# Optimization experiments

Measured on AMD Instinct MI355X. Metric: run time of the kernel, lower is better.

Reference implementation:

```python
import jax, jax.numpy as jnp
import numpy as np

N_NODES = 150000  # n_users + n_items
N_EDGES = 2400000
D = 128
LEAKY_SLOPE = 0.2  # tf.nn.leaky_relu default alpha
L2_EPS = 1e-12     # tf.math.l2_normalize epsilon


def setup_inputs() -> dict:
    key = jax.random.key(0)
    ks = jax.random.split(key, 8)
    edge_row = jax.random.randint(ks[0], (N_EDGES,), 0, N_NODES, dtype=jnp.int32)
    edge_col = jax.random.randint(ks[1], (N_EDGES,), 0, N_NODES, dtype=jnp.int32)
    edge_val = jax.random.uniform(ks[2], (N_EDGES,), dtype=jnp.float32)
    ego_embeddings = jax.random.normal(ks[3], (N_NODES, D), dtype=jnp.float32)
    w_gc = jax.random.normal(ks[4], (D, D), dtype=jnp.float32) * 0.05
    b_gc = jax.random.normal(ks[5], (D,), dtype=jnp.float32) * 0.05
    w_bi = jax.random.normal(ks[6], (D, D), dtype=jnp.float32) * 0.05
    b_bi = jax.random.normal(ks[7], (D,), dtype=jnp.float32) * 0.05
    return {"edge_row": edge_row, "edge_col": edge_col, "edge_val": edge_val,
            "ego_embeddings": ego_embeddings,
            "w_gc": w_gc, "b_gc": b_gc, "w_bi": w_bi, "b_bi": b_bi}


def reference(edge_row, edge_col, edge_val, ego_embeddings, w_gc, b_gc, w_bi, b_bi):
    # Sparse A @ ego  (concat over n_fold row-blocks == full SpMM)
    msgs = edge_val[:, None] * ego_embeddings[edge_col]          # [E, D]
    side = jax.ops.segment_sum(msgs, edge_row, num_segments=N_NODES)  # [N, D]
    # dual dense transform + leaky_relu
    sum_emb = jax.nn.leaky_relu(side @ w_gc + b_gc, negative_slope=LEAKY_SLOPE)
    bi_emb = jax.nn.leaky_relu((ego_embeddings * side) @ w_bi + b_bi,
                               negative_slope=LEAKY_SLOPE)
    ego = sum_emb + bi_emb
    # dropout rate = 1 - mess_dropout = 0 -> identity (deterministic)
    # tf.math.l2_normalize(axis=1)
    sq = jnp.sum(ego * ego, axis=1, keepdims=True)
    norm_emb = ego * jax.lax.rsqrt(jnp.maximum(sq, L2_EPS))
    return norm_emb
```

## Files before the change

### kernel.cpp

```cpp
#include <hip/hip_runtime.h>
#include <hip/hip_bf16.h>

constexpr int N_NODES = 150000;
constexpr int N_EDGES = 2400000;
constexpr int D       = 128;
constexpr float LEAKY = 0.2f;
constexpr float L2EPS = 1e-12f;

constexpr int NB_SCAN = (N_NODES + 255) / 256;

constexpr int RB_LOG = 9;
constexpr int RB     = 1 << RB_LOG;
constexpr int NBK    = (N_NODES + RB - 1) >> RB_LOG;
constexpr int EPT_A  = 32;
constexpr int EPB_A  = 256 * EPT_A;

typedef short  short8  __attribute__((ext_vector_type(8)));
typedef short  short4v __attribute__((ext_vector_type(4)));
typedef float  f32x4   __attribute__((ext_vector_type(4)));

static __device__ __forceinline__ short f2bf(float x) {
  __hip_bfloat16 h = __float2bfloat16(x);
  return *reinterpret_cast<short*>(&h);
}

__global__ __launch_bounds__(256) void bucket_hist_kernel(
    const int* __restrict__ erow, int* __restrict__ bkt_cnt) {
  __shared__ int h[NBK];
  const int t = threadIdx.x;
  for (int i = t; i < NBK; i += 256) h[i] = 0;
  __syncthreads();
  const long long e0 = (long long)blockIdx.x * EPB_A;
  #pragma unroll
  for (int k = 0; k < EPT_A; ++k) {
    long long e = e0 + k * 256 + t;
    if (e < N_EDGES) atomicAdd(&h[erow[e] >> RB_LOG], 1);
  }
  __syncthreads();
  for (int i = t; i < NBK; i += 256) {
    int c = h[i];
    if (c) atomicAdd(&bkt_cnt[i], c);
  }
}

__global__ __launch_bounds__(512) void bucket_scan_kernel(
    const int* __restrict__ bkt_cnt,
    int* __restrict__ bbase,
    int* __restrict__ bcur,
    int* __restrict__ offs) {
  __shared__ int s[512];
  const int t = threadIdx.x;
  int v = (t < NBK) ? bkt_cnt[t] : 0;
  s[t] = v;
  __syncthreads();
  for (int off = 1; off < 512; off <<= 1) {
    int tmp = (t >= off) ? s[t - off] : 0;
    __syncthreads();
    s[t] += tmp;
    __syncthreads();
  }
  if (t < NBK) {
    int excl = s[t] - v;
    bbase[t] = excl;
    bcur[t]  = excl;
  }
  if (t == 0) { bbase[NBK] = N_EDGES; offs[N_NODES] = N_EDGES; }
}

__global__ __launch_bounds__(256) void hist_kernel(
    const int* __restrict__ erow, int* __restrict__ cnt) {
  int base = blockIdx.x * 2048 + threadIdx.x;
  #pragma unroll
  for (int k = 0; k < 8; ++k) {
    int e = base + k * 256;
    if (e < N_EDGES) atomicAdd(&cnt[erow[e]], 1);
  }
}

__global__ __launch_bounds__(256) void scan_block_sums(
    const int* __restrict__ cnt, int* __restrict__ bsums) {
  __shared__ int s[256];
  int i = blockIdx.x * 256 + threadIdx.x;
  s[threadIdx.x] = (i < N_NODES) ? cnt[i] : 0;
  __syncthreads();
  for (int off = 128; off > 0; off >>= 1) {
    if (threadIdx.x < off) s[threadIdx.x] += s[threadIdx.x + off];
    __syncthreads();
  }
  if (threadIdx.x == 0) bsums[blockIdx.x] = s[0];
}

__global__ __launch_bounds__(1024) void scan_partials(int* __restrict__ bsums) {
  __shared__ int s[1024];
  int v = (threadIdx.x < NB_SCAN) ? bsums[threadIdx.x] : 0;
  s[threadIdx.x] = v;
  __syncthreads();
  for (int off = 1; off < 1024; off <<= 1) {
    int t = (threadIdx.x >= off) ? s[threadIdx.x - off] : 0;
    __syncthreads();
    s[threadIdx.x] += t;
    __syncthreads();
  }
  if (threadIdx.x < NB_SCAN) bsums[threadIdx.x] = s[threadIdx.x] - v;
}

__global__ __launch_bounds__(256) void scan_final(
    const int* __restrict__ cnt, const int* __restrict__ bsums,
    int* __restrict__ offs, int* __restrict__ cursor) {
  __shared__ int s[256];
  int i = blockIdx.x * 256 + threadIdx.x;
  int v = (i < N_NODES) ? cnt[i] : 0;
  s[threadIdx.x] = v;
  __syncthreads();
  for (int off = 1; off < 256; off <<= 1) {
    int t = (threadIdx.x >= off) ? s[threadIdx.x - off] : 0;
    __syncthreads();
    s[threadIdx.x] += t;
    __syncthreads();
  }
  if (i < N_NODES) {
    int excl = s[threadIdx.x] - v + bsums[blockIdx.x];
    offs[i]   = excl;
    cursor[i] = excl;
  }
  if (i == 0) offs[N_NODES] = N_EDGES;
}

__global__ __launch_bounds__(256) void bucket_scatter_kernel(
    const int*   __restrict__ erow,
    const int*   __restrict__ ecol,
    const float* __restrict__ eval,
    int*         __restrict__ bcur,
    int2*        __restrict__ stage) {
  __shared__ int h[NBK];
  __shared__ int basea[NBK];
  const int t = threadIdx.x;
  const long long e0 = (long long)blockIdx.x * EPB_A;

  for (int i = t; i < NBK; i += 256) h[i] = 0;
  __syncthreads();

  int rows[EPT_A];
  #pragma unroll
  for (int k = 0; k < EPT_A; ++k) {
    long long e = e0 + k * 256 + t;
    int r = -1;
    if (e < N_EDGES) { r = erow[e]; atomicAdd(&h[r >> RB_LOG], 1); }
    rows[k] = r;
  }
  __syncthreads();

  for (int b = t; b < NBK; b += 256) {
    int c = h[b];
    basea[b] = c ? atomicAdd(&bcur[b], c) : 0;
    h[b] = 0;
  }
  __syncthreads();

  #pragma unroll
  for (int k = 0; k < EPT_A; ++k) {
    int r = rows[k];
    if (r >= 0) {
      long long e = e0 + k * 256 + t;
      int bkt  = r >> RB_LOG;
      int rank = atomicAdd(&h[bkt], 1);
      int pos  = basea[bkt] + rank;
      int pack = ecol[e] | ((r & (RB - 1)) << 18);
      stage[pos] = make_int2(pack, __float_as_int(eval[e]));
    }
  }
}

__global__ __launch_bounds__(256) void bucket_permute_kernel(
    const int*  __restrict__ bbase,
    const int2* __restrict__ stage,
    int2*       __restrict__ ev,
    int*        __restrict__ offs) {
  __shared__ int cnt[RB];
  __shared__ int s[256];
  const int t    = threadIdx.x;
  const int bkt  = blockIdx.x;
  const int row0 = bkt << RB_LOG;
  const int w0   = bbase[bkt];
  const int w1   = bbase[bkt + 1];

  for (int i = t; i < RB; i += 256) cnt[i] = 0;
  __syncthreads();

  for (int i = w0 + t; i < w1; i += 256) {
    int px = ((const int*)stage)[2 * (size_t)i];
    atomicAdd(&cnt[(px >> 18) & (RB - 1)], 1);
  }
  __syncthreads();

  int c0 = cnt[2 * t], c1 = cnt[2 * t + 1];
  int pairsum = c0 + c1;
  s[t] = pairsum;
  __syncthreads();
  for (int off = 1; off < 256; off <<= 1) {
    int v = (t >= off) ? s[t - off] : 0;
    __syncthreads();
    s[t] += v;
    __syncthreads();
  }
  int pexcl = s[t] - pairsum;
  int e0 = w0 + pexcl;
  int e1 = e0 + c0;
  cnt[2 * t]     = e0;
  cnt[2 * t + 1] = e1;
  int r0 = row0 + 2 * t;
  if (r0 < N_NODES)     offs[r0]     = e0;
  if (r0 + 1 < N_NODES) offs[r0 + 1] = e1;
  __syncthreads();

  for (int i = w0 + t; i < w1; i += 256) {
    int2 e = stage[i];
    int rl  = (e.x >> 18) & (RB - 1);
    int pos = atomicAdd(&cnt[rl], 1);
    ev[pos] = make_int2(e.x & 0x3FFFF, e.y);
  }
}

__global__ __launch_bounds__(256) void bin_kernel(
    const int*   __restrict__ erow,
    const int*   __restrict__ ecol,
    const float* __restrict__ eval,
    int*         __restrict__ cursor,
    int2*        __restrict__ sorted_ev) {
  int base = blockIdx.x * 1024 + threadIdx.x;
  int e0 = base, e1 = base + 256, e2 = base + 512, e3 = base + 768;
  int r0 = (e0 < N_EDGES) ? erow[e0] : 0;
  int r1 = (e1 < N_EDGES) ? erow[e1] : 0;
  int r2 = (e2 < N_EDGES) ? erow[e2] : 0;
  int r3 = (e3 < N_EDGES) ? erow[e3] : 0;
  int p0 = (e0 < N_EDGES) ? atomicAdd(&cursor[r0], 1) : 0;
  int p1 = (e1 < N_EDGES) ? atomicAdd(&cursor[r1], 1) : 0;
  int p2 = (e2 < N_EDGES) ? atomicAdd(&cursor[r2], 1) : 0;
  int p3 = (e3 < N_EDGES) ? atomicAdd(&cursor[r3], 1) : 0;
  if (e0 < N_EDGES) sorted_ev[p0] = make_int2(ecol[e0], __float_as_int(eval[e0]));
  if (e1 < N_EDGES) sorted_ev[p1] = make_int2(ecol[e1], __float_as_int(eval[e1]));
  if (e2 < N_EDGES) sorted_ev[p2] = make_int2(ecol[e2], __float_as_int(eval[e2]));
  if (e3 < N_EDGES) sorted_ev[p3] = make_int2(ecol[e3], __float_as_int(eval[e3]));
}

__global__ __launch_bounds__(256) void conv_ego_kernel(
    const float* __restrict__ ego, short* __restrict__ ebf) {
  int i = blockIdx.x * 256 + threadIdx.x;
  constexpr int TOTAL = N_NODES * D / 4;
  if (i < TOTAL) {
    float4 v = ((const float4*)ego)[i];
    short4v p;
    p[0] = f2bf(v.x); p[1] = f2bf(v.y); p[2] = f2bf(v.z); p[3] = f2bf(v.w);
    ((short4v*)ebf)[i] = p;
  }
}

__global__ __launch_bounds__(128) void prep_weights_kernel(
    const float* __restrict__ wg, const float* __restrict__ wb,
    short* __restrict__ wtg, short* __restrict__ wtb) {
  int n = blockIdx.x;
  int k = threadIdx.x;
  wtg[n * D + k] = f2bf(wg[k * D + n]);
  wtb[n * D + k] = f2bf(wb[k * D + n]);
}

__global__ __launch_bounds__(256) void spmm_transform_kernel(
    const int*   __restrict__ offs,
    const int2*  __restrict__ ev,
    const short* __restrict__ ebf,
    const float* __restrict__ ego,
    const short* __restrict__ wtg,
    const short* __restrict__ wtb,
    const float* __restrict__ b_gc,
    const float* __restrict__ b_bi,
    float*       __restrict__ out) {
  __shared__ short sA[16][136];
  __shared__ short sP[16][136];
  __shared__ float sO[16][132];
  __shared__ float sInv[16];

  const int t    = threadIdx.x;
  const int g    = t >> 4;
  const int lg   = t & 15;
  const int base = blockIdx.x * 16;
  const int row  = base + g;

  const int s0 = offs[row], s1 = offs[row + 1];
  float a0 = 0.f, a1 = 0.f, a2 = 0.f, a3 = 0.f;
  float a4 = 0.f, a5 = 0.f, a6 = 0.f, a7 = 0.f;

  auto accum = [&](int2 e) {
    uint4 u = *(const uint4*)(ebf + (size_t)e.x * D + lg * 8);
    float v = __int_as_float(e.y);
    a0 = fmaf(v, __uint_as_float(u.x << 16), a0);
    a1 = fmaf(v, __uint_as_float(u.x & 0xffff0000u), a1);
    a2 = fmaf(v, __uint_as_float(u.y << 16), a2);
    a3 = fmaf(v, __uint_as_float(u.y & 0xffff0000u), a3);
    a4 = fmaf(v, __uint_as_float(u.z << 16), a4);
    a5 = fmaf(v, __uint_as_float(u.z & 0xffff0000u), a5);
    a6 = fmaf(v, __uint_as_float(u.w << 16), a6);
    a7 = fmaf(v, __uint_as_float(u.w & 0xffff0000u), a7);
  };

  int i = s0;
  const int n4 = s0 + ((s1 - s0) & ~3);
  for (; i < n4; i += 4) {
    int2 e0 = ev[i], e1 = ev[i + 1], e2 = ev[i + 2], e3 = ev[i + 3];
    accum(e0); accum(e1); accum(e2); accum(e3);
  }
  for (; i < s1; ++i) accum(ev[i]);

  {
    const float* er = ego + (size_t)row * D + lg * 8;
    float4 ev0 = *(const float4*)(er);
    float4 ev1 = *(const float4*)(er + 4);
    short4v pa0, pa1, pp0, pp1;
    pa0[0] = f2bf(a0); pa0[1] = f2bf(a1); pa0[2] = f2bf(a2); pa0[3] = f2bf(a3);
    pa1[0] = f2bf(a4); pa1[1] = f2bf(a5); pa1[2] = f2bf(a6); pa1[3] = f2bf(a7);
    pp0[0] = f2bf(a0 * ev0.x); pp0[1] = f2bf(a1 * ev0.y);
    pp0[2] = f2bf(a2 * ev0.z); pp0[3] = f2bf(a3 * ev0.w);
    pp1[0] = f2bf(a4 * ev1.x); pp1[1] = f2bf(a5 * ev1.y);
    pp1[2] = f2bf(a6 * ev1.z); pp1[3] = f2bf(a7 * ev1.w);
    *(short4v*)&sA[g][lg * 8]     = pa0;
    *(short4v*)&sA[g][lg * 8 + 4] = pa1;
    *(short4v*)&sP[g][lg * 8]     = pp0;
    *(short4v*)&sP[g][lg * 8 + 4] = pp1;
  }
  __syncthreads();

  {
    const int w    = t >> 6;
    const int l64  = t & 63;
    const int arow = l64 & 15;
    const int koff = (l64 >> 4) * 8;
    const int nb   = w * 32;

    f32x4 accg[2] = {{0.f, 0.f, 0.f, 0.f}, {0.f, 0.f, 0.f, 0.f}};
    f32x4 accb[2] = {{0.f, 0.f, 0.f, 0.f}, {0.f, 0.f, 0.f, 0.f}};

    #pragma unroll
    for (int ks = 0; ks < 4; ++ks) {
      const int k0 = ks * 32 + koff;
      short8 a_s = *(const short8*)&sA[arow][k0];
      short8 a_p = *(const short8*)&sP[arow][k0];
      #pragma unroll
      for (int ct = 0; ct < 2; ++ct) {
        const int n = nb + ct * 16 + arow;
        short8 bgf = *(const short8*)(wtg + (size_t)n * D + k0);
        short8 bbf = *(const short8*)(wtb + (size_t)n * D + k0);
        accg[ct] = __builtin_amdgcn_mfma_f32_16x16x32_bf16(a_s, bgf, accg[ct], 0, 0, 0);
        accb[ct] = __builtin_amdgcn_mfma_f32_16x16x32_bf16(a_p, bbf, accb[ct], 0, 0, 0);
      }
    }

    #pragma unroll
    for (int ct = 0; ct < 2; ++ct) {
      const int col = nb + ct * 16 + arow;
      const float bg = b_gc[col];
      const float bb = b_bi[col];
      #pragma unroll
      for (int j = 0; j < 4; ++j) {
        const int r = (l64 >> 4) * 4 + j;
        float x1 = accg[ct][j] + bg; x1 = (x1 > 0.f) ? x1 : LEAKY * x1;
        float x2 = accb[ct][j] + bb; x2 = (x2 > 0.f) ? x2 : LEAKY * x2;
        sO[r][col] = x1 + x2;
      }
    }
  }
  __syncthreads();

  {
    const int r = t >> 4, c16 = t & 15;
    float sum = 0.f;
    #pragma unroll
    for (int i2 = 0; i2 < 8; ++i2) {
      float v = sO[r][c16 * 8 + i2];
      sum = fmaf(v, v, sum);
    }
    #pragma unroll
    for (int off = 8; off > 0; off >>= 1) sum += __shfl_down(sum, off, 16);
    if (c16 == 0) sInv[r] = rsqrtf(fmaxf(sum, L2EPS));
  }
  __syncthreads();

  #pragma unroll
  for (int k = 0; k < 2; ++k) {
    int f  = k * 256 + t;
    int r  = f >> 5;
    int c4 = (f & 31) * 4;
    float inv = sInv[r];
    float4 v = *(const float4*)&sO[r][c4];
    v.x *= inv; v.y *= inv; v.z *= inv; v.w *= inv;
    *(float4*)(out + (size_t)(base + r) * D + c4) = v;
  }
}

__global__ __launch_bounds__(256) void spmm_kernel(
    const int*  __restrict__ offs,
    const int2* __restrict__ ev,
    const float* __restrict__ ego,
    float*       __restrict__ side) {
  const int t = threadIdx.x;
  const int g = t >> 5;
  const int l = t & 31;
  const int row = blockIdx.x * 8 + g;
  if (row >= N_NODES) return;
  const int s0 = offs[row], s1 = offs[row + 1];
  float ax = 0.f, ay = 0.f, az = 0.f, aw = 0.f;
  int i = s0;
  const int n4 = s0 + ((s1 - s0) & ~3);
  for (; i < n4; i += 4) {
    int2 e0 = ev[i], e1 = ev[i + 1], e2 = ev[i + 2], e3 = ev[i + 3];
    float4 g0 = *(const float4*)(ego + (size_t)e0.x * D + 4 * l);
    float4 g1 = *(const float4*)(ego + (size_t)e1.x * D + 4 * l);
    float4 g2 = *(const float4*)(ego + (size_t)e2.x * D + 4 * l);
    float4 g3 = *(const float4*)(ego + (size_t)e3.x * D + 4 * l);
    float v0 = __int_as_float(e0.y), v1 = __int_as_float(e1.y);
    float v2 = __int_as_float(e2.y), v3 = __int_as_float(e3.y);
    ax = fmaf(v0, g0.x, ax); ay = fmaf(v0, g0.y, ay);
    az = fmaf(v0, g0.z, az); aw = fmaf(v0, g0.w, aw);
    ax = fmaf(v1, g1.x, ax); ay = fmaf(v1, g1.y, ay);
    az = fmaf(v1, g1.z, az); aw = fmaf(v1, g1.w, aw);
    ax = fmaf(v2, g2.x, ax); ay = fmaf(v2, g2.y, ay);
    az = fmaf(v2, g2.z, az); aw = fmaf(v2, g2.w, aw);
    ax = fmaf(v3, g3.x, ax); ay = fmaf(v3, g3.y, ay);
    az = fmaf(v3, g3.z, az); aw = fmaf(v3, g3.w, aw);
  }
  for (; i < s1; ++i) {
    int2 e = ev[i];
    float4 gg = *(const float4*)(ego + (size_t)e.x * D + 4 * l);
    float v = __int_as_float(e.y);
    ax = fmaf(v, gg.x, ax); ay = fmaf(v, gg.y, ay);
    az = fmaf(v, gg.z, az); aw = fmaf(v, gg.w, aw);
  }
  *(float4*)(side + (size_t)row * D + 4 * l) = make_float4(ax, ay, az, aw);
}

__global__ __launch_bounds__(256) void transform_mfma_kernel(
    const float* __restrict__ side,
    const float* __restrict__ ego,
    const short* __restrict__ wtg,
    const short* __restrict__ wtb,
    const float* __restrict__ b_gc,
    const float* __restrict__ b_bi,
    float*       __restrict__ out) {
  __shared__ short sA[16][136];
  __shared__ short sP[16][136];
  __shared__ float sO[16][132];
  __shared__ float sInv[16];

  const int t    = threadIdx.x;
  const int w    = t >> 6;
  const int l    = t & 63;
  const int base = blockIdx.x * 16;

  #pragma unroll
  for (int k = 0; k < 2; ++k) {
    int f  = k * 256 + t;
    int r  = f >> 5;
    int c4 = (f & 31) * 4;
    float4 sv = *(const float4*)(side + (size_t)(base + r) * D + c4);
    float4 ev = *(const float4*)(ego  + (size_t)(base + r) * D + c4);
    short4v pa, pp;
    pa[0] = f2bf(sv.x); pa[1] = f2bf(sv.y); pa[2] = f2bf(sv.z); pa[3] = f2bf(sv.w);
    pp[0] = f2bf(sv.x * ev.x); pp[1] = f2bf(sv.y * ev.y);
    pp[2] = f2bf(sv.z * ev.z); pp[3] = f2bf(sv.w * ev.w);
    *(short4v*)&sA[r][c4] = pa;
    *(short4v*)&sP[r][c4] = pp;
  }
  __syncthreads();

  f32x4 accg[2] = {{0.f, 0.f, 0.f, 0.f}, {0.f, 0.f, 0.f, 0.f}};
  f32x4 accb[2] = {{0.f, 0.f, 0.f, 0.f}, {0.f, 0.f, 0.f, 0.f}};

  const int arow = l & 15;
  const int koff = (l >> 4) * 8;
  const int nb   = w * 32;

  #pragma unroll
  for (int ks = 0; ks < 4; ++ks) {
    const int k0 = ks * 32 + koff;
    short8 a_s = *(const short8*)&sA[arow][k0];
    short8 a_p = *(const short8*)&sP[arow][k0];
    #pragma unroll
    for (int ct = 0; ct < 2; ++ct) {
      const int n = nb + ct * 16 + arow;
      short8 bgf = *(const short8*)(wtg + (size_t)n * D + k0);
      short8 bbf = *(const short8*)(wtb + (size_t)n * D + k0);
      accg[ct] = __builtin_amdgcn_mfma_f32_16x16x32_bf16(a_s, bgf, accg[ct], 0, 0, 0);
      accb[ct] = __builtin_amdgcn_mfma_f32_16x16x32_bf16(a_p, bbf, accb[ct], 0, 0, 0);
    }
  }

  #pragma unroll
  for (int ct = 0; ct < 2; ++ct) {
    const int col = nb + ct * 16 + arow;
    const float bg = b_gc[col];
    const float bb = b_bi[col];
    #pragma unroll
    for (int j = 0; j < 4; ++j) {
      const int r = (l >> 4) * 4 + j;
      float x1 = accg[ct][j] + bg; x1 = (x1 > 0.f) ? x1 : LEAKY * x1;
      float x2 = accb[ct][j] + bb; x2 = (x2 > 0.f) ? x2 : LEAKY * x2;
      sO[r][col] = x1 + x2;
    }
  }
  __syncthreads();

  {
    const int r = t >> 4, c16 = t & 15;
    float sum = 0.f;
    #pragma unroll
    for (int i = 0; i < 8; ++i) {
      float v = sO[r][c16 * 8 + i];
      sum = fmaf(v, v, sum);
    }
    #pragma unroll
    for (int off = 8; off > 0; off >>= 1) sum += __shfl_down(sum, off, 16);
    if (c16 == 0) sInv[r] = rsqrtf(fmaxf(sum, L2EPS));
  }
  __syncthreads();

  #pragma unroll
  for (int k = 0; k < 2; ++k) {
    int f  = k * 256 + t;
    int r  = f >> 5;
    int c4 = (f & 31) * 4;
    float inv = sInv[r];
    float4 v = *(const float4*)&sO[r][c4];
    v.x *= inv; v.y *= inv; v.z *= inv; v.w *= inv;
    *(float4*)(out + (size_t)(base + r) * D + c4) = v;
  }
}

__global__ __launch_bounds__(256) void scatter_kernel(
    const int*   __restrict__ erow,
    const int*   __restrict__ ecol,
    const float* __restrict__ eval,
    const float* __restrict__ ego,
    float*       __restrict__ side) {
  long long t = (long long)blockIdx.x * blockDim.x + threadIdx.x;
  int e = (int)(t >> 5);
  if (e >= N_EDGES) return;
  int c = (int)(t & 31);
  int r  = erow[e];
  int cl = ecol[e];
  float v = eval[e];
  const float4* src = (const float4*)(ego + (long long)cl * D);
  float4 m = src[c];
  float* dst = side + (long long)r * D + c * 4;
  atomicAdd(dst + 0, v * m.x);
  atomicAdd(dst + 1, v * m.y);
  atomicAdd(dst + 2, v * m.z);
  atomicAdd(dst + 3, v * m.w);
}

__global__ __launch_bounds__(128) void transform_f32_kernel(
    const float* __restrict__ side,
    const float* __restrict__ ego,
    const float* __restrict__ w_gc,
    const float* __restrict__ b_gc,
    const float* __restrict__ w_bi,
    const float* __restrict__ b_bi,
    float*       __restrict__ out) {
  constexpr int RPB = 16;
  __shared__ float s_side[RPB][D];
  __shared__ float s_prod[RPB][D];
  __shared__ float s_part[RPB][2];
  const int j    = threadIdx.x;
  const int base = blockIdx.x * RPB;
  #pragma unroll
  for (int r = 0; r < RPB; ++r) {
    int node = base + r;
    float s = 0.f, e = 0.f;
    if (node < N_NODES) {
      s = side[(long long)node * D + j];
      e = ego [(long long)node * D + j];
    }
    s_side[r][j] = s;
    s_prod[r][j] = e * s;
  }
  __syncthreads();
  float acc_gc[RPB], acc_bi[RPB];
  #pragma unroll
  for (int r = 0; r < RPB; ++r) { acc_gc[r] = 0.f; acc_bi[r] = 0.f; }
  for (int k = 0; k < D; ++k) {
    float wg = w_gc[k * D + j];
    float wb = w_bi[k * D + j];
    #pragma unroll
    for (int r = 0; r < RPB; ++r) {
      acc_gc[r] = fmaf(s_side[r][k], wg, acc_gc[r]);
      acc_bi[r] = fmaf(s_prod[r][k], wb, acc_bi[r]);
    }
  }
  const float bg = b_gc[j];
  const float bb = b_bi[j];
  #pragma unroll
  for (int r = 0; r < RPB; ++r) {
    float x1 = acc_gc[r] + bg; x1 = (x1 > 0.f) ? x1 : LEAKY * x1;
    float x2 = acc_bi[r] + bb; x2 = (x2 > 0.f) ? x2 : LEAKY * x2;
    acc_gc[r] = x1 + x2;
  }
  const int lane = j & 63;
  const int wv   = j >> 6;
  #pragma unroll
  for (int r = 0; r < RPB; ++r) {
    float sq = acc_gc[r] * acc_gc[r];
    #pragma unroll
    for (int off = 32; off > 0; off >>= 1) sq += __shfl_down(sq, off, 64);
    if (lane == 0) s_part[r][wv] = sq;
  }
  __syncthreads();
  #pragma unroll
  for (int r = 0; r < RPB; ++r) {
    int node = base + r;
    if (node < N_NODES) {
      float tot = s_part[r][0] + s_part[r][1];
      float inv = rsqrtf(fmaxf(tot, L2EPS));
      out[(long long)node * D + j] = acc_gc[r] * inv;
    }
  }
}

extern "C" void kernel_launch(void* const* d_in, const int* in_sizes, int n_in,
                              void* d_out, int out_size, void* d_ws, size_t ws_size,
                              hipStream_t stream) {
  const int*   erow = (const int*)  d_in[0];
  const int*   ecol = (const int*)  d_in[1];
  const float* eval = (const float*)d_in[2];
  const float* ego  = (const float*)d_in[3];
  const float* w_gc = (const float*)d_in[4];
  const float* b_gc = (const float*)d_in[5];
  const float* w_bi = (const float*)d_in[6];
  const float* b_bi = (const float*)d_in[7];
  float* out = (float*)d_out;

  auto align256 = [](size_t x) { return (x + 255) & ~(size_t)255; };
  size_t off_cnt    = 0;
  size_t off_offs   = align256(off_cnt    + (size_t)N_NODES * 4);
  size_t off_cursor = align256(off_offs   + (size_t)(N_NODES + 1) * 4);
  size_t off_bsums  = align256(off_cursor + (size_t)N_NODES * 4);
  size_t off_bcur   = align256(off_bsums  + 1024 * 4);
  size_t off_wtg    = align256(off_bcur   + (size_t)NBK * 4);
  size_t off_wtb    = align256(off_wtg    + (size_t)D * D * 2);
  size_t off_ev     = align256(off_wtb    + (size_t)D * D * 2);
  size_t off_ebf    = align256(off_ev     + (size_t)N_EDGES * 8);
  size_t ws_mid     = off_ebf;
  size_t ws_sort    = off_ebf + (size_t)N_EDGES * 8;
  size_t ws_full    = off_ebf + (size_t)N_NODES * D * 2;

  if (ws_size >= ws_mid) {
    char* ws = (char*)d_ws;
    int*   cnt    = (int*)  (ws + off_cnt);
    int*   offs   = (int*)  (ws + off_offs);
    int*   cursor = (int*)  (ws + off_cursor);
    int*   bsums  = (int*)  (ws + off_bsums);
    int*   bcur   = (int*)  (ws + off_bcur);
    short* wtg    = (short*)(ws + off_wtg);
    short* wtb    = (short*)(ws + off_wtb);
    int2*  ev     = (int2*) (ws + off_ev);
    short* ebf    = (short*)(ws + off_ebf);
    int2*  stage  = (int2*) (ws + off_ebf);

    bool bucketed = (ws_size >= ws_sort);
    if (bucketed) {
      hipMemsetAsync(cnt, 0, (size_t)NBK * 4, stream);
      bucket_hist_kernel<<<(N_EDGES + EPB_A - 1) / EPB_A, 256, 0, stream>>>(erow, cnt);
      bucket_scan_kernel<<<1, 512, 0, stream>>>(cnt, bsums, bcur, offs);
      bucket_scatter_kernel<<<(N_EDGES + EPB_A - 1) / EPB_A, 256, 0, stream>>>(
          erow, ecol, eval, bcur, stage);
      bucket_permute_kernel<<<NBK, 256, 0, stream>>>(bsums, stage, ev, offs);
    } else {
      hipMemsetAsync(cnt, 0, (size_t)N_NODES * 4, stream);
      hist_kernel<<<(N_EDGES + 2047) / 2048, 256, 0, stream>>>(erow, cnt);
      scan_block_sums<<<NB_SCAN, 256, 0, stream>>>(cnt, bsums);
      scan_partials<<<1, 1024, 0, stream>>>(bsums);
      scan_final<<<NB_SCAN, 256, 0, stream>>>(cnt, bsums, offs, cursor);
      bin_kernel<<<(N_EDGES + 1023) / 1024, 256, 0, stream>>>(
          erow, ecol, eval, cursor, ev);
    }
    prep_weights_kernel<<<D, D, 0, stream>>>(w_gc, w_bi, wtg, wtb);

    if (ws_size >= ws_full) {
      conv_ego_kernel<<<(N_NODES * D / 4 + 255) / 256, 256, 0, stream>>>(ego, ebf);
      spmm_transform_kernel<<<N_NODES / 16, 256, 0, stream>>>(
          offs, ev, ebf, ego, wtg, wtb, b_gc, b_bi, out);
    } else {
      float* side = out;
      spmm_kernel<<<(N_NODES + 7) / 8, 256, 0, stream>>>(offs, ev, ego, side);
      transform_mfma_kernel<<<N_NODES / 16, 256, 0, stream>>>(
          side, ego, wtg, wtb, b_gc, b_bi, out);
    }
  } else {
    float* side = out;
    hipMemsetAsync(side, 0, (size_t)N_NODES * D * 4, stream);
    long long total = (long long)N_EDGES * 32;
    int grid = (int)((total + 255) / 256);
    scatter_kernel<<<grid, 256, 0, stream>>>(erow, ecol, eval, ego, side);
    transform_f32_kernel<<<N_NODES / 16, 128, 0, stream>>>(
        side, ego, w_gc, b_gc, w_bi, b_bi, out);
  }
}
```

Measured before the change: 409.8 us.

## Balance fused SpMM edges across 16-row block with LDS atomic row reduction

The fused SpMM+transform kernel now splits the block's total edge range evenly across its 16 thread groups instead of giving each group one row. Row identity is kept in the packed edge word, and partial sums are flushed into shared memory with atomics whenever the row changes. This targets load imbalance from varying row degrees, at the cost of LDS zeroing, extra syncs, atomic flushes and masking of the column index.

New measurement: 483.7 us. +18.0%, slower.

```diff
diff --git a/kernel.cpp b/kernel.cpp
--- a/kernel.cpp
+++ b/kernel.cpp
@@ -217,7 +217,7 @@
     int2 e = stage[i];
     int rl  = (e.x >> 18) & (RB - 1);
     int pos = atomicAdd(&cnt[rl], 1);
-    ev[pos] = make_int2(e.x & 0x3FFFF, e.y);
+    ev[pos] = e;
   }
 }
 
@@ -283,15 +283,36 @@
   const int g    = t >> 4;
   const int lg   = t & 15;
   const int base = blockIdx.x * 16;
-  const int row  = base + g;
-
-  const int s0 = offs[row], s1 = offs[row + 1];
+
+  #pragma unroll
+  for (int k = 0; k < 8; ++k) {
+    int idx = k * 256 + t;
+    sO[idx >> 7][idx & 127] = 0.f;
+  }
+  __syncthreads();
+
+  const int W0 = offs[base], W1 = offs[base + 16];
+  const int chunk = ((W1 - W0) + 15) >> 4;
+  const int cbeg = W0 + g * chunk;
+  const int cend = min(cbeg + chunk, W1);
+
+  const short* ebl = ebf + lg * 8;
+
   float a0 = 0.f, a1 = 0.f, a2 = 0.f, a3 = 0.f;
   float a4 = 0.f, a5 = 0.f, a6 = 0.f, a7 = 0.f;
-
-  auto accum = [&](int2 e) {
-    uint4 u = *(const uint4*)(ebf + (size_t)e.x * D + lg * 8);
-    float v = __int_as_float(e.y);
+  int cur = -1;
+
+  auto flush = [&]() {
+    if (cur >= 0) {
+      float* dst = &sO[cur][lg * 8];
+      atomicAdd(dst + 0, a0); atomicAdd(dst + 1, a1);
+      atomicAdd(dst + 2, a2); atomicAdd(dst + 3, a3);
+      atomicAdd(dst + 4, a4); atomicAdd(dst + 5, a5);
+      atomicAdd(dst + 6, a6); atomicAdd(dst + 7, a7);
+    }
+    a0 = a1 = a2 = a3 = a4 = a5 = a6 = a7 = 0.f;
+  };
+  auto accum = [&](uint4 u, float v) {
     a0 = fmaf(v, __uint_as_float(u.x << 16), a0);
     a1 = fmaf(v, __uint_as_float(u.x & 0xffff0000u), a1);
     a2 = fmaf(v, __uint_as_float(u.y << 16), a2);
@@ -302,25 +323,49 @@
     a7 = fmaf(v, __uint_as_float(u.w & 0xffff0000u), a7);
   };
 
-  int i = s0;
-  const int n4 = s0 + ((s1 - s0) & ~3);
+  int i = cbeg;
+  const int n4 = cbeg + ((cend - cbeg) & ~3);
   for (; i < n4; i += 4) {
-    int2 e0 = ev[i], e1 = ev[i + 1], e2 = ev[i + 2], e3 = ev[i + 3];
-    accum(e0); accum(e1); accum(e2); accum(e3);
-  }
-  for (; i < s1; ++i) accum(ev[i]);
+    int2 e0 = ev[i + 0], e1 = ev[i + 1], e2 = ev[i + 2], e3 = ev[i + 3];
+    uint4 u0 = *(const uint4*)(ebl + (size_t)(e0.x & 0x3FFFF) * D);
+    uint4 u1 = *(const uint4*)(ebl + (size_t)(e1.x & 0x3FFFF) * D);
+    uint4 u2 = *(const uint4*)(ebl + (size_t)(e2.x & 0x3FFFF) * D);
+    uint4 u3 = *(const uint4*)(ebl + (size_t)(e3.x & 0x3FFFF) * D);
+    int r0 = (e0.x >> 18) & 15, r1 = (e1.x >> 18) & 15;
+    int r2 = (e2.x >> 18) & 15, r3 = (e3.x >> 18) & 15;
+    if (r0 != cur) { flush(); cur = r0; }
+    accum(u0, __int_as_float(e0.y));
+    if (r1 != cur) { flush(); cur = r1; }
+    accum(u1, __int_as_float(e1.y));
+    if (r2 != cur) { flush(); cur = r2; }
+    accum(u2, __int_as_float(e2.y));
+    if (r3 != cur) { flush(); cur = r3; }
+    accum(u3, __int_as_float(e3.y));
+  }
+  for (; i < cend; ++i) {
+    int2 e = ev[i];
+    uint4 u = *(const uint4*)(ebl + (size_t)(e.x & 0x3FFFF) * D);
+    int r = (e.x >> 18) & 15;
+    if (r != cur) { flush(); cur = r; }
+    accum(u, __int_as_float(e.y));
+  }
+  flush();
+  __syncthreads();
 
   {
+    const int row = base + g;
+    float4 v0 = *(const float4*)&sO[g][lg * 8];
+    float4 v1 = *(const float4*)&sO[g][lg * 8 + 4];
     const float* er = ego + (size_t)row * D + lg * 8;
-    float4 ev0 = *(const float4*)(er);
-    float4 ev1 = *(const float4*)(er + 4);
+    float4 e0v = *(const float4*)(er);
+    float4 e1v = *(const float4*)(er + 4);
     short4v pa0, pa1, pp0, pp1;
-    pa0[0] = f2bf(a0); pa0[1] = f2bf(a1); pa0[2] = f2bf(a2); pa0[3] = f2bf(a3);
-    pa1[0] = f2bf(a4); pa1[1] = f2bf(a5); pa1[2] = f2bf(a6); pa1[3] = f2bf(a7);
-    pp0[0] = f2bf(a0 * ev0.x); pp0[1] = f2bf(a1 * ev0.y);
-    pp0[2] = f2bf(a2 * ev0.z); pp0[3] = f2bf(a3 * ev0.w);
-    pp1[0] = f2bf(a4 * ev1.x); pp1[1] = f2bf(a5 * ev1.y);
-    pp1[2] = f2bf(a6 * ev1.z); pp1[3] = f2bf(a7 * ev1.w);
+    pa0[0] = f2bf(v0.x); pa0[1] = f2bf(v0.y); pa0[2] = f2bf(v0.z); pa0[3] = f2bf(v0.w);
+    pa1[0] = f2bf(v1.x); pa1[1] = f2bf(v1.y); pa1[2] = f2bf(v1.z); pa1[3] = f2bf(v1.w);
+    pp0[0] = f2bf(v0.x * e0v.x); pp0[1] = f2bf(v0.y * e0v.y);
+    pp0[2] = f2bf(v0.z * e0v.z); pp0[3] = f2bf(v0.w * e0v.w);
+    pp1[0] = f2bf(v1.x * e1v.x); pp1[1] = f2bf(v1.y * e1v.y);
+    pp1[2] = f2bf(v1.z * e1v.z); pp1[3] = f2bf(v1.w * e1v.w);
     *(short4v*)&sA[g][lg * 8]     = pa0;
     *(short4v*)&sA[g][lg * 8 + 4] = pa1;
     *(short4v*)&sP[g][lg * 8]     = pp0;
@@ -411,10 +456,10 @@
   const int n4 = s0 + ((s1 - s0) & ~3);
   for (; i < n4; i += 4) {
     int2 e0 = ev[i], e1 = ev[i + 1], e2 = ev[i + 2], e3 = ev[i + 3];
-    float4 g0 = *(const float4*)(ego + (size_t)e0.x * D + 4 * l);
-    float4 g1 = *(const float4*)(ego + (size_t)e1.x * D + 4 * l);
-    float4 g2 = *(const float4*)(ego + (size_t)e2.x * D + 4 * l);
-    float4 g3 = *(const float4*)(ego + (size_t)e3.x * D + 4 * l);
+    float4 g0 = *(const float4*)(ego + (size_t)(e0.x & 0x3FFFF) * D + 4 * l);
+    float4 g1 = *(const float4*)(ego + (size_t)(e1.x & 0x3FFFF) * D + 4 * l);
+    float4 g2 = *(const float4*)(ego + (size_t)(e2.x & 0x3FFFF) * D + 4 * l);
+    float4 g3 = *(const float4*)(ego + (size_t)(e3.x & 0x3FFFF) * D + 4 * l);
     float v0 = __int_as_float(e0.y), v1 = __int_as_float(e1.y);
     float v2 = __int_as_float(e2.y), v3 = __int_as_float(e3.y);
     ax = fmaf(v0, g0.x, ax); ay = fmaf(v0, g0.y, ay);
@@ -428,7 +473,7 @@
   }
   for (; i < s1; ++i) {
     int2 e = ev[i];
-    float4 gg = *(const float4*)(ego + (size_t)e.x * D + 4 * l);
+    float4 gg = *(const float4*)(ego + (size_t)(e.x & 0x3FFFF) * D + 4 * l);
     float v = __int_as_float(e.y);
     ax = fmaf(v, gg.x, ax); ay = fmaf(v, gg.y, ay);
     az = fmaf(v, gg.z, az); aw = fmaf(v, gg.w, aw);
```
